# Kernel tuning notes

Measured on AMD Instinct MI355X. Metric: run time of the kernel, lower is better.

Reference implementation:

```python
import jax, jax.numpy as jnp
import numpy as np

M, K, N = 8192, 4096, 4096

def setup_inputs() -> dict:
    key = jax.random.key(0)
    k1, k2, k3, k4, k5, k6 = jax.random.split(key, 6)
    # quantized activations (per-token symmetric int8)
    x_q = jax.random.randint(k1, (M, K), -128, 128, dtype=jnp.int32).astype(jnp.int8)
    # quantized weight (asymmetric per-output-channel): w_fp16 = scale_weight * (w_q + zp_weight)
    weight = jax.random.randint(k2, (N, K), -128, 128, dtype=jnp.int32).astype(jnp.int8)
    scale_input = (jax.random.uniform(k3, (M,), jnp.float32) * 0.009 + 0.001).astype(jnp.float16)
    scale_weight = (jax.random.uniform(k4, (N,), jnp.float32) * 0.009 + 0.001).astype(jnp.float16)
    zp_weight = jax.random.randint(k5, (N,), 100, 156, dtype=jnp.int32).astype(jnp.int16)
    bias = (jax.random.normal(k6, (N,), jnp.float32) * 0.01).astype(jnp.float16)
    # per-row sum of quantized activations (needed for zero-point correction)
    sum_input = jnp.sum(x_q.astype(jnp.int32), axis=-1).astype(jnp.float32)
    return {
        "input": x_q,
        "weight": weight,
        "bias": bias,
        "scale_input": scale_input,
        "scale_weight": scale_weight,
        "sum_input": sum_input,
        "zp_weight": zp_weight,
    }

def reference(input, weight, bias, scale_input, scale_weight, sum_input, zp_weight):
    acc = jnp.matmul(input.astype(jnp.int32), weight.astype(jnp.int32).T)
    # asymmetric weight zero-point correction: + zp_n * sum_k(x_q[m, k])
    corr = sum_input[:, None] * zp_weight.astype(jnp.float32)[None, :]
    # fused dequant epilogue: per-row activation scale * per-col weight scale, + bias
    scale = scale_input.astype(jnp.float32)[:, None] * scale_weight.astype(jnp.float32)[None, :]
    out = (acc.astype(jnp.float32) + corr) * scale + bias.astype(jnp.float32)[None, :]
    return out.astype(jnp.float16)
```

## Files before the change

kernel.cpp:

```cpp
#include <hip/hip_runtime.h>
#include <hip/hip_bf16.h>
#include <stdint.h>


#define BM 128
#define BN 128
#define BK 64

typedef __attribute__((ext_vector_type(4))) int int32x4;

__device__ __forceinline__ void async_copy16(const uint8_t* g, uint8_t* l) {
  __builtin_amdgcn_global_load_lds(
      (const __attribute__((address_space(1))) uint32_t*)(const void*)g,
      (__attribute__((address_space(3))) uint32_t*)l,
      16, 0, 0);
}

__global__ __launch_bounds__(256) void pack_kernel(
    const int* __restrict__ A, const int* __restrict__ B,
    uint8_t* __restrict__ A8, uint8_t* __restrict__ B8,
    int nA16, int nTot16) {
  int t = blockIdx.x * blockDim.x + threadIdx.x;
  if (t >= nTot16) return;
  const int4* src;
  uint4* dst;
  if (t < nA16) {
    src = (const int4*)A + (size_t)t * 4;
    dst = (uint4*)A8 + t;
  } else {
    int u = t - nA16;
    src = (const int4*)B + (size_t)u * 4;
    dst = (uint4*)B8 + u;
  }
  uint32_t w[4];
#pragma unroll
  for (int q = 0; q < 4; ++q) {
    int4 v = src[q];
    w[q] = (uint32_t)(v.x & 255) | ((uint32_t)(v.y & 255) << 8) |
           ((uint32_t)(v.z & 255) << 16) | ((uint32_t)(v.w & 255) << 24);
  }
  *dst = make_uint4(w[0], w[1], w[2], w[3]);
}

template <bool PACKED>
__global__ __launch_bounds__(256) void w8a8_gemm(
    const uint8_t* __restrict__ A8, const uint8_t* __restrict__ B8,
    const int* __restrict__ A32, const int* __restrict__ B32,
    const float* __restrict__ bias,
    const float* __restrict__ s_in,
    const float* __restrict__ s_w,
    const float* __restrict__ sum_in,
    const int* __restrict__ zp_w,
    float* __restrict__ out,
    int M, int N, int K) {
  __shared__ uint8_t As[BM * BK];
  __shared__ uint8_t Bs[BN * BK];

  const int tid = threadIdx.x;
  const int bm = blockIdx.y, bn = blockIdx.x;
  const int row0 = bm * BM, col0 = bn * BN;
  const int wave = tid >> 6, lane = tid & 63;
  const int quad = lane >> 4, r = lane & 15;
  const int wm = (wave >> 1) * 64, wn = (wave & 1) * 64;

  const int lin = tid * 16;
  const int srow = lin >> 6;
  const int scol = lin & 63;
  const size_t sK = (size_t)K;

  int32x4 acc[4][4] = {};

  for (int k0 = 0; k0 < K; k0 += BK) {
    if (PACKED) {
      const uint8_t* ag = A8 + (size_t)(row0 + srow) * sK + k0 + scol;
      const uint8_t* bg = B8 + (size_t)(col0 + srow) * sK + k0 + scol;
      async_copy16(ag, &As[lin]);
      async_copy16(ag + 64 * sK, &As[lin + 4096]);
      async_copy16(bg, &Bs[lin]);
      async_copy16(bg + 64 * sK, &Bs[lin + 4096]);
    } else {
#pragma unroll
      for (int c = 0; c < 2; ++c) {
        const int* ag = A32 + (size_t)(row0 + srow + c * 64) * sK + k0 + scol;
        const int* bg = B32 + (size_t)(col0 + srow + c * 64) * sK + k0 + scol;
        int32x4 pa, pb;
#pragma unroll
        for (int q = 0; q < 4; ++q) {
          int4 va = ((const int4*)ag)[q];
          int4 vb = ((const int4*)bg)[q];
          pa[q] = (int)((uint32_t)(va.x & 255) | ((uint32_t)(va.y & 255) << 8) |
                        ((uint32_t)(va.z & 255) << 16) | ((uint32_t)(va.w & 255) << 24));
          pb[q] = (int)((uint32_t)(vb.x & 255) | ((uint32_t)(vb.y & 255) << 8) |
                        ((uint32_t)(vb.z & 255) << 16) | ((uint32_t)(vb.w & 255) << 24));
        }
        *(int32x4*)&As[lin + c * 4096] = pa;
        *(int32x4*)&Bs[lin + c * 4096] = pb;
      }
    }
    __syncthreads();

    int32x4 afrag[4], bfrag[4];
#pragma unroll
    for (int i = 0; i < 4; ++i)
      afrag[i] = *(const int32x4*)&As[(wm + i * 16 + r) * 64 + quad * 16];
#pragma unroll
    for (int j = 0; j < 4; ++j)
      bfrag[j] = *(const int32x4*)&Bs[(wn + j * 16 + r) * 64 + quad * 16];
#pragma unroll
    for (int i = 0; i < 4; ++i)
#pragma unroll
      for (int j = 0; j < 4; ++j)
        acc[i][j] = __builtin_amdgcn_mfma_i32_16x16x64_i8(afrag[i], bfrag[j],
                                                          acc[i][j], 0, 0, 0);
    __syncthreads();
  }

  float swj[4], zpj[4], bj[4];
#pragma unroll
  for (int j = 0; j < 4; ++j) {
    int gc = col0 + wn + j * 16 + r;
    swj[j] = s_w[gc];
    zpj[j] = (float)zp_w[gc];
    bj[j] = bias[gc];
  }
#pragma unroll
  for (int i = 0; i < 4; ++i) {
#pragma unroll
    for (int t = 0; t < 4; ++t) {
      int gr = row0 + wm + i * 16 + quad * 4 + t;
      float siv = s_in[gr];
      float suv = sum_in[gr];
      float* orow = out + (size_t)gr * N + col0 + wn + r;
#pragma unroll
      for (int j = 0; j < 4; ++j) {
        float v = ((float)acc[i][j][t] + suv * zpj[j]) * (siv * swj[j]) + bj[j];
        orow[j * 16] = v;
      }
    }
  }
}

extern "C" void kernel_launch(void* const* d_in, const int* in_sizes, int n_in,
                              void* d_out, int out_size, void* d_ws, size_t ws_size,
                              hipStream_t stream) {
  const int* x_q = (const int*)d_in[0];
  const int* w_q = (const int*)d_in[1];
  const float* bias = (const float*)d_in[2];
  const float* s_in = (const float*)d_in[3];
  const float* s_w = (const float*)d_in[4];
  const float* sum_in = (const float*)d_in[5];
  const int* zp_w = (const int*)d_in[6];
  float* out = (float*)d_out;

  const int M = in_sizes[3];
  const int N = in_sizes[2];
  const int K = in_sizes[0] / M;

  const size_t needA = (size_t)M * K;
  const size_t needB = (size_t)N * K;
  dim3 grid(N / BN, M / BM), block(256);

  if (ws_size >= needA + needB) {
    uint8_t* A8 = (uint8_t*)d_ws;
    uint8_t* B8 = A8 + needA;
    const int nA16 = (int)(needA / 16);
    const int nTot16 = (int)((needA + needB) / 16);
    pack_kernel<<<(nTot16 + 255) / 256, 256, 0, stream>>>(x_q, w_q, A8, B8,
                                                          nA16, nTot16);
    w8a8_gemm<true><<<grid, block, 0, stream>>>(A8, B8, nullptr, nullptr, bias,
                                                s_in, s_w, sum_in, zp_w, out,
                                                M, N, K);
  } else {
    w8a8_gemm<false><<<grid, block, 0, stream>>>(nullptr, nullptr, x_q, w_q,
                                                 bias, s_in, s_w, sum_in, zp_w,
                                                 out, M, N, K);
  }
}
```

Measured before the change: 468.1 us.

## Double BK to 128 with XOR-swizzled LDS layout and finer-grained pack kernel

The GEMM K-tile grows from 64 to 128, which halves the number of barrier pairs per tile. Async global-to-LDS copies now use an XOR-swizzled column-group layout so that fragment reads avoid LDS bank conflicts. The pack kernel has each thread convert one int4 to one uint32 instead of four, which gives more parallel and better coalesced conversion. The unpacked path moves into a separate fallback kernel, and LDS use doubles to 32KB per block, which may lower occupancy.

```diff
diff --git a/kernel.cpp b/kernel.cpp
--- a/kernel.cpp
+++ b/kernel.cpp
@@ -5,7 +5,7 @@
 
 #define BM 128
 #define BN 128
-#define BK 64
+#define BK 128
 
 typedef __attribute__((ext_vector_type(4))) int int32x4;
 
@@ -19,33 +19,26 @@
 __global__ __launch_bounds__(256) void pack_kernel(
     const int* __restrict__ A, const int* __restrict__ B,
     uint8_t* __restrict__ A8, uint8_t* __restrict__ B8,
-    int nA16, int nTot16) {
+    int nA4, int nTot4) {
   int t = blockIdx.x * blockDim.x + threadIdx.x;
-  if (t >= nTot16) return;
+  if (t >= nTot4) return;
   const int4* src;
-  uint4* dst;
-  if (t < nA16) {
-    src = (const int4*)A + (size_t)t * 4;
-    dst = (uint4*)A8 + t;
+  uint32_t* dst;
+  if (t < nA4) {
+    src = (const int4*)A + t;
+    dst = (uint32_t*)A8 + t;
   } else {
-    int u = t - nA16;
-    src = (const int4*)B + (size_t)u * 4;
-    dst = (uint4*)B8 + u;
-  }
-  uint32_t w[4];
-#pragma unroll
-  for (int q = 0; q < 4; ++q) {
-    int4 v = src[q];
-    w[q] = (uint32_t)(v.x & 255) | ((uint32_t)(v.y & 255) << 8) |
-           ((uint32_t)(v.z & 255) << 16) | ((uint32_t)(v.w & 255) << 24);
-  }
-  *dst = make_uint4(w[0], w[1], w[2], w[3]);
-}
-
-template <bool PACKED>
+    int u = t - nA4;
+    src = (const int4*)B + u;
+    dst = (uint32_t*)B8 + u;
+  }
+  int4 v = *src;
+  *dst = (uint32_t)(v.x & 255) | ((uint32_t)(v.y & 255) << 8) |
+         ((uint32_t)(v.z & 255) << 16) | ((uint32_t)(v.w & 255) << 24);
+}
+
 __global__ __launch_bounds__(256) void w8a8_gemm(
     const uint8_t* __restrict__ A8, const uint8_t* __restrict__ B8,
-    const int* __restrict__ A32, const int* __restrict__ B32,
     const float* __restrict__ bias,
     const float* __restrict__ s_in,
     const float* __restrict__ s_w,
@@ -62,43 +55,112 @@
   const int wave = tid >> 6, lane = tid & 63;
   const int quad = lane >> 4, r = lane & 15;
   const int wm = (wave >> 1) * 64, wn = (wave & 1) * 64;
-
+  const size_t sK = (size_t)K;
+
+  const int row_s = tid >> 3;
+  const int cg = (tid & 7) ^ ((tid >> 4) & 7);
+  const int ldst = tid * 16;
+
+  int32x4 acc[4][4] = {};
+
+  for (int k0 = 0; k0 < K; k0 += BK) {
+#pragma unroll
+    for (int p = 0; p < 4; ++p) {
+      const int rr = p * 32 + row_s;
+      async_copy16(A8 + (size_t)(row0 + rr) * sK + k0 + cg * 16,
+                   &As[p * 4096 + ldst]);
+      async_copy16(B8 + (size_t)(col0 + rr) * sK + k0 + cg * 16,
+                   &Bs[p * 4096 + ldst]);
+    }
+    __syncthreads();
+
+#pragma unroll
+    for (int s = 0; s < 2; ++s) {
+      int32x4 afrag[4], bfrag[4];
+      const int swzr = (r >> 1) & 7;
+      const int cslot = ((s * 4 + quad) ^ swzr) * 16;
+#pragma unroll
+      for (int i = 0; i < 4; ++i)
+        afrag[i] = *(const int32x4*)&As[(wm + i * 16 + r) * BK + cslot];
+#pragma unroll
+      for (int j = 0; j < 4; ++j)
+        bfrag[j] = *(const int32x4*)&Bs[(wn + j * 16 + r) * BK + cslot];
+#pragma unroll
+      for (int i = 0; i < 4; ++i)
+#pragma unroll
+        for (int j = 0; j < 4; ++j)
+          acc[i][j] = __builtin_amdgcn_mfma_i32_16x16x64_i8(
+              afrag[i], bfrag[j], acc[i][j], 0, 0, 0);
+    }
+    __syncthreads();
+  }
+
+  float swj[4], zpj[4], bj[4];
+#pragma unroll
+  for (int j = 0; j < 4; ++j) {
+    int gc = col0 + wn + j * 16 + r;
+    swj[j] = s_w[gc];
+    zpj[j] = (float)zp_w[gc];
+    bj[j] = bias[gc];
+  }
+#pragma unroll
+  for (int i = 0; i < 4; ++i) {
+#pragma unroll
+    for (int t = 0; t < 4; ++t) {
+      int gr = row0 + wm + i * 16 + quad * 4 + t;
+      float siv = s_in[gr];
+      float suv = sum_in[gr];
+      float* orow = out + (size_t)gr * N + col0 + wn + r;
+#pragma unroll
+      for (int j = 0; j < 4; ++j) {
+        float v = ((float)acc[i][j][t] + suv * zpj[j]) * (siv * swj[j]) + bj[j];
+        orow[j * 16] = v;
+      }
+    }
+  }
+}
+
+__global__ __launch_bounds__(256) void w8a8_gemm_fallback(
+    const int* __restrict__ A32, const int* __restrict__ B32,
+    const float* __restrict__ bias,
+    const float* __restrict__ s_in,
+    const float* __restrict__ s_w,
+    const float* __restrict__ sum_in,
+    const int* __restrict__ zp_w,
+    float* __restrict__ out,
+    int M, int N, int K) {
+  __shared__ uint8_t As[128 * 64];
+  __shared__ uint8_t Bs[128 * 64];
+  const int tid = threadIdx.x;
+  const int bm = blockIdx.y, bn = blockIdx.x;
+  const int row0 = bm * 128, col0 = bn * 128;
+  const int wave = tid >> 6, lane = tid & 63;
+  const int quad = lane >> 4, r = lane & 15;
+  const int wm = (wave >> 1) * 64, wn = (wave & 1) * 64;
   const int lin = tid * 16;
   const int srow = lin >> 6;
   const int scol = lin & 63;
   const size_t sK = (size_t)K;
-
   int32x4 acc[4][4] = {};
-
-  for (int k0 = 0; k0 < K; k0 += BK) {
-    if (PACKED) {
-      const uint8_t* ag = A8 + (size_t)(row0 + srow) * sK + k0 + scol;
-      const uint8_t* bg = B8 + (size_t)(col0 + srow) * sK + k0 + scol;
-      async_copy16(ag, &As[lin]);
-      async_copy16(ag + 64 * sK, &As[lin + 4096]);
-      async_copy16(bg, &Bs[lin]);
-      async_copy16(bg + 64 * sK, &Bs[lin + 4096]);
-    } else {
-#pragma unroll
-      for (int c = 0; c < 2; ++c) {
-        const int* ag = A32 + (size_t)(row0 + srow + c * 64) * sK + k0 + scol;
-        const int* bg = B32 + (size_t)(col0 + srow + c * 64) * sK + k0 + scol;
-        int32x4 pa, pb;
-#pragma unroll
-        for (int q = 0; q < 4; ++q) {
-          int4 va = ((const int4*)ag)[q];
-          int4 vb = ((const int4*)bg)[q];
-          pa[q] = (int)((uint32_t)(va.x & 255) | ((uint32_t)(va.y & 255) << 8) |
-                        ((uint32_t)(va.z & 255) << 16) | ((uint32_t)(va.w & 255) << 24));
-          pb[q] = (int)((uint32_t)(vb.x & 255) | ((uint32_t)(vb.y & 255) << 8) |
-                        ((uint32_t)(vb.z & 255) << 16) | ((uint32_t)(vb.w & 255) << 24));
-        }
-        *(int32x4*)&As[lin + c * 4096] = pa;
-        *(int32x4*)&Bs[lin + c * 4096] = pb;
+  for (int k0 = 0; k0 < K; k0 += 64) {
+#pragma unroll
+    for (int c = 0; c < 2; ++c) {
+      const int* ag = A32 + (size_t)(row0 + srow + c * 64) * sK + k0 + scol;
+      const int* bg = B32 + (size_t)(col0 + srow + c * 64) * sK + k0 + scol;
+      int32x4 pa, pb;
+#pragma unroll
+      for (int q = 0; q < 4; ++q) {
+        int4 va = ((const int4*)ag)[q];
+        int4 vb = ((const int4*)bg)[q];
+        pa[q] = (int)((uint32_t)(va.x & 255) | ((uint32_t)(va.y & 255) << 8) |
+                      ((uint32_t)(va.z & 255) << 16) | ((uint32_t)(va.w & 255) << 24));
+        pb[q] = (int)((uint32_t)(vb.x & 255) | ((uint32_t)(vb.y & 255) << 8) |
+                      ((uint32_t)(vb.z & 255) << 16) | ((uint32_t)(vb.w & 255) << 24));
       }
-    }
-    __syncthreads();
-
+      *(int32x4*)&As[lin + c * 4096] = pa;
+      *(int32x4*)&Bs[lin + c * 4096] = pb;
+    }
+    __syncthreads();
     int32x4 afrag[4], bfrag[4];
 #pragma unroll
     for (int i = 0; i < 4; ++i)
@@ -114,7 +176,6 @@
                                                           acc[i][j], 0, 0, 0);
     __syncthreads();
   }
-
   float swj[4], zpj[4], bj[4];
 #pragma unroll
   for (int j = 0; j < 4; ++j) {
@@ -163,16 +224,14 @@
   if (ws_size >= needA + needB) {
     uint8_t* A8 = (uint8_t*)d_ws;
     uint8_t* B8 = A8 + needA;
-    const int nA16 = (int)(needA / 16);
-    const int nTot16 = (int)((needA + needB) / 16);
-    pack_kernel<<<(nTot16 + 255) / 256, 256, 0, stream>>>(x_q, w_q, A8, B8,
-                                                          nA16, nTot16);
-    w8a8_gemm<true><<<grid, block, 0, stream>>>(A8, B8, nullptr, nullptr, bias,
-                                                s_in, s_w, sum_in, zp_w, out,
-                                                M, N, K);
+    const int nA4 = (int)(needA / 4);
+    const int nTot4 = (int)((needA + needB) / 4);
+    pack_kernel<<<(nTot4 + 255) / 256, 256, 0, stream>>>(x_q, w_q, A8, B8,
+                                                         nA4, nTot4);
+    w8a8_gemm<<<grid, block, 0, stream>>>(A8, B8, bias, s_in, s_w, sum_in,
+                                          zp_w, out, M, N, K);
   } else {
-    w8a8_gemm<false><<<grid, block, 0, stream>>>(nullptr, nullptr, x_q, w_q,
-                                                 bias, s_in, s_w, sum_in, zp_w,
-                                                 out, M, N, K);
-  }
-}
+    w8a8_gemm_fallback<<<grid, block, 0, stream>>>(x_q, w_q, bias, s_in, s_w,
+                                                   sum_in, zp_w, out, M, N, K);
+  }
+}
```

Measured after the change: 422.0 us. 1.11x faster.
